# Kernel tuning notes

Measured on AMD Instinct MI355X. Metric: run time of the kernel, lower is better.

The kernel has to match this reference:

```python
import jax, jax.numpy as jnp
import numpy as np

N = 50000          # nodes
E = 800000         # edges (avg degree 16)
F = 128            # in_dim = num_hidden*heads = pred_dim
H = 4              # attention heads per layer
D = 32             # num_hidden (per-head dim)
R = 11             # rel_num
L = 2              # num_layers
SCALE = float(1.0 / np.sqrt(D))


def setup_inputs() -> dict:
    key = jax.random.key(0)
    ks = jax.random.split(key, 16)
    inputs = jax.random.normal(ks[0], (N, F), jnp.float32)
    edge_types = jax.random.randint(ks[1], (E,), 0, R)
    src = jax.random.randint(ks[2], (E,), 0, N)
    dst = jax.random.randint(ks[3], (E,), 0, N)
    centrality = jax.random.uniform(ks[4], (N,), jnp.float32)
    rel_emb = jax.random.normal(ks[5], (R, F), jnp.float32) * 0.1
    # stacked per-layer projection weights (both layers have F -> H*D = F)
    Wq = jax.random.normal(ks[6], (L, F, H * D), jnp.float32) * 0.05
    Wk = jax.random.normal(ks[7], (L, F, H * D), jnp.float32) * 0.05
    Wv = jax.random.normal(ks[8], (L, F, H * D), jnp.float32) * 0.05
    We = jax.random.normal(ks[9], (L, F, H * D), jnp.float32) * 0.05
    bq = jnp.zeros((L, H * D), jnp.float32)
    bk = jnp.zeros((L, H * D), jnp.float32)
    bv = jnp.zeros((L, H * D), jnp.float32)
    be = jnp.zeros((L, H * D), jnp.float32)
    W_out = jax.random.normal(ks[10], (H * D, 1), jnp.float32) * 0.05
    b_out = jnp.zeros((1,), jnp.float32)
    gamma = jnp.ones((1,), jnp.float32)
    beta = jnp.zeros((1,), jnp.float32)
    return {"inputs": inputs, "edge_types": edge_types, "src": src, "dst": dst,
            "centrality": centrality, "rel_emb": rel_emb,
            "Wq": Wq, "bq": bq, "Wk": Wk, "bk": bk, "Wv": Wv, "bv": bv,
            "We": We, "be": be, "W_out": W_out, "b_out": b_out,
            "gamma": gamma, "beta": beta}


def _segment_softmax(score, dst, n):
    # score: [E, H]; softmax over incoming edges of each dst node
    m = jax.ops.segment_max(score, dst, num_segments=n)          # [N, H]
    ex = jnp.exp(score - m[dst])                                  # [E, H]
    s = jax.ops.segment_sum(ex, dst, num_segments=n)              # [N, H]
    return ex / (s[dst] + 1e-9)


def reference(inputs, edge_types, src, dst, centrality, rel_emb,
              Wq, bq, Wk, bk, Wv, bv, We, be, W_out, b_out, gamma, beta):
    h = inputs                                   # [N, F]
    ef = rel_emb[edge_types]                     # [E, pred_dim] relational edge embedding
    for l in range(L):
        q = (h @ Wq[l] + bq[l]).reshape(N, H, D)
        k = (h @ Wk[l] + bk[l]).reshape(N, H, D)
        v = (h @ Wv[l] + bv[l]).reshape(N, H, D)
        e = (ef @ We[l] + be[l]).reshape(E, H, D)
        # edge_mode="add": edge features added to keys/values on each edge
        ke = k[src] + e                           # [E, H, D]
        score = jnp.sum(q[dst] * ke, axis=-1) * SCALE   # [E, H]
        attn = _segment_softmax(score, dst, N)          # [E, H]
        msg = attn[:, :, None] * (v[src] + e)           # [E, H, D]
        agg = jax.ops.segment_sum(msg, dst, num_segments=N)  # [N, H, D]
        # identity residual (in_dim == H*D) + ELU activation
        h = jax.nn.elu(agg.reshape(N, H * D) + h)
    logits = h @ W_out + b_out                    # [N, 1]
    logits = jax.nn.relu((centrality * gamma + beta)[:, None] * logits)
    return logits
```

## Files before the change

kernel.cpp:

```cpp
#include <hip/hip_runtime.h>
#include <hip/hip_bf16.h>
#include <math.h>

#define SCALE_C 0.17677669529663687f
#define CAPP 64

typedef short bf16x8 __attribute__((ext_vector_type(8)));
typedef float f32x4 __attribute__((ext_vector_type(4)));


__global__ __launch_bounds__(256) void prep_scatter_k(
    const float* __restrict__ Wq, const float* __restrict__ Wk, const float* __restrict__ Wv,
    __hip_bfloat16* __restrict__ wf,
    const float* __restrict__ rel_emb, const float* __restrict__ We, const float* __restrict__ be,
    float* __restrict__ re, int R, int reb,
    const int* __restrict__ dst, const int* __restrict__ src, const int* __restrict__ etype,
    int E, int* __restrict__ cnt, int* __restrict__ bins) {
  int b = blockIdx.x;
  if (b < 48) {
    int tid = b * 256 + threadIdx.x;
    int lane = tid & 63;
    int frag = tid >> 6;
    int ks = frag & 3;
    int ct = (frag >> 2) & 7;
    int mat = frag >> 5;
    int l = mat / 3, m = mat % 3;
    const float* W = ((m == 0) ? Wq : (m == 1) ? Wk : Wv) + (size_t)l * 128 * 128;
    int nn = ct * 16 + (lane & 15);
    int k0 = ks * 32 + (lane >> 4) * 8;
    __hip_bfloat16 tmp[8];
    #pragma unroll
    for (int j = 0; j < 8; ++j) tmp[j] = __float2bfloat16(W[(size_t)(k0 + j) * 128 + nn]);
    *(uint4*)&wf[(size_t)frag * 64 * 8 + (size_t)lane * 8] = *(const uint4*)tmp;
  } else if (b < 48 + reb) {
    int idx = (b - 48) * 256 + threadIdx.x;
    int tot = 2 * R * 128;
    if (idx >= tot) return;
    int c = idx & 127;
    int r = (idx >> 7) % R;
    int l = idx / (R * 128);
    const float* W = We + (size_t)l * 128 * 128;
    float acc = be[l * 128 + c];
    #pragma unroll 4
    for (int kk = 0; kk < 128; ++kk) acc += rel_emb[r * 128 + kk] * W[kk * 128 + c];
    re[idx] = acc;
  } else {
    int e = (b - 48 - reb) * 256 + threadIdx.x;
    if (e < E) {
      int d = dst[e];
      int pos = atomicAdd(&cnt[d], 1);
      if (pos < CAPP) bins[(d << 6) + pos] = src[e] | (etype[e] << 20);
    }
  }
}


__device__ __forceinline__ void qkv_body(
    const float* __restrict__ Xf, const __hip_bfloat16* __restrict__ Xb,
    const __hip_bfloat16* __restrict__ wf,
    const float* __restrict__ bq, const float* __restrict__ bk, const float* __restrict__ bv,
    __hip_bfloat16* __restrict__ qo, __hip_bfloat16* __restrict__ kvo, int n, int bid) {
  __shared__ __hip_bfloat16 kvt[2][32][264];
  int wid = threadIdx.x >> 6;
  int lane = threadIdx.x & 63;
  int row0 = bid * 64 + wid * 32;
  if (row0 >= n) return;
  int cl = lane & 15;
  int quad = lane >> 4;

  bf16x8 afrag[2][4];
  #pragma unroll
  for (int s = 0; s < 2; ++s) {
    int arow = row0 + s * 16 + cl;
    bool av = arow < n;
    if (Xb) {
      const __hip_bfloat16* xr = Xb + (size_t)arow * 128 + quad * 8;
      #pragma unroll
      for (int ks = 0; ks < 4; ++ks) {
        uint4 raw = av ? *(const uint4*)(xr + ks * 32) : make_uint4(0, 0, 0, 0);
        afrag[s][ks] = __builtin_bit_cast(bf16x8, raw);
      }
    } else {
      const float* xr = Xf + (size_t)arow * 128 + quad * 8;
      #pragma unroll
      for (int ks = 0; ks < 4; ++ks) {
        float4 x0 = av ? *(const float4*)(xr + ks * 32)     : make_float4(0.f, 0.f, 0.f, 0.f);
        float4 x1 = av ? *(const float4*)(xr + ks * 32 + 4) : make_float4(0.f, 0.f, 0.f, 0.f);
        union { bf16x8 v; __hip_bfloat16 h[8]; } fu;
        fu.h[0] = __float2bfloat16(x0.x); fu.h[1] = __float2bfloat16(x0.y);
        fu.h[2] = __float2bfloat16(x0.z); fu.h[3] = __float2bfloat16(x0.w);
        fu.h[4] = __float2bfloat16(x1.x); fu.h[5] = __float2bfloat16(x1.y);
        fu.h[6] = __float2bfloat16(x1.z); fu.h[7] = __float2bfloat16(x1.w);
        afrag[s][ks] = fu.v;
      }
    }
  }
  const uint4* wfu = (const uint4*)wf;

  #pragma unroll
  for (int ct = 0; ct < 8; ++ct) {
    f32x4 a0 = {0.f, 0.f, 0.f, 0.f}, a1 = {0.f, 0.f, 0.f, 0.f};
    #pragma unroll
    for (int ks = 0; ks < 4; ++ks) {
      uint4 braw = wfu[((size_t)ct * 4 + ks) * 64 + lane];
      bf16x8 bfr = __builtin_bit_cast(bf16x8, braw);
      a0 = __builtin_amdgcn_mfma_f32_16x16x32_bf16(afrag[0][ks], bfr, a0, 0, 0, 0);
      a1 = __builtin_amdgcn_mfma_f32_16x16x32_bf16(afrag[1][ks], bfr, a1, 0, 0, 0);
    }
    int c = ct * 16 + cl;
    float bb = bq[c];
    #pragma unroll
    for (int r = 0; r < 4; ++r) {
      kvt[wid][quad * 4 + r][c]      = __float2bfloat16((a0[r] + bb) * SCALE_C);
      kvt[wid][16 + quad * 4 + r][c] = __float2bfloat16((a1[r] + bb) * SCALE_C);
    }
  }
  {
    const uint4* tsrc = (const uint4*)&kvt[wid][0][0];
    #pragma unroll
    for (int it = 0; it < 8; ++it) {
      int idx = it * 64 + lane;
      int row = idx >> 4, g = idx & 15;
      if (row0 + row < n)
        *(uint4*)&qo[((size_t)(row0 + row)) * 128 + g * 8] = tsrc[row * 33 + g];
    }
  }

  #pragma unroll
  for (int m = 1; m <= 2; ++m) {
    const float* bias = (m == 1) ? bk : bv;
    #pragma unroll
    for (int ct = 0; ct < 8; ++ct) {
      f32x4 a0 = {0.f, 0.f, 0.f, 0.f}, a1 = {0.f, 0.f, 0.f, 0.f};
      #pragma unroll
      for (int ks = 0; ks < 4; ++ks) {
        uint4 braw = wfu[((size_t)(m * 8 + ct) * 4 + ks) * 64 + lane];
        bf16x8 bfr = __builtin_bit_cast(bf16x8, braw);
        a0 = __builtin_amdgcn_mfma_f32_16x16x32_bf16(afrag[0][ks], bfr, a0, 0, 0, 0);
        a1 = __builtin_amdgcn_mfma_f32_16x16x32_bf16(afrag[1][ks], bfr, a1, 0, 0, 0);
      }
      int c = ct * 16 + cl;
      float bb = bias[c];
      int p = 8 * (c >> 2) + (c & 3) + ((m == 2) ? 4 : 0);
      #pragma unroll
      for (int r = 0; r < 4; ++r) {
        kvt[wid][quad * 4 + r][p]      = __float2bfloat16(a0[r] + bb);
        kvt[wid][16 + quad * 4 + r][p] = __float2bfloat16(a1[r] + bb);
      }
    }
  }
  {
    const uint4* tsrc = (const uint4*)&kvt[wid][0][0];
    #pragma unroll
    for (int it = 0; it < 16; ++it) {
      int idx = it * 64 + lane;
      int row = idx >> 5, off = idx & 31;
      if (row0 + row < n)
        *(uint4*)&kvo[((size_t)(row0 + row)) * 256 + off * 8] = tsrc[row * 33 + off];
    }
  }
}

__global__ __launch_bounds__(128) void qkv1_k(
    const float* __restrict__ Xf, const __hip_bfloat16* __restrict__ wf,
    const float* __restrict__ bq, const float* __restrict__ bk, const float* __restrict__ bv,
    __hip_bfloat16* __restrict__ qo, __hip_bfloat16* __restrict__ kvo, int n) {
  qkv_body(Xf, nullptr, wf, bq, bk, bv, qo, kvo, n, blockIdx.x);
}

__global__ __launch_bounds__(128) void qkv2_k(
    const __hip_bfloat16* __restrict__ Xb, const __hip_bfloat16* __restrict__ wf,
    const float* __restrict__ bq, const float* __restrict__ bk, const float* __restrict__ bv,
    __hip_bfloat16* __restrict__ qo, __hip_bfloat16* __restrict__ kvo, int n) {
  qkv_body(nullptr, Xb, wf, bq, bk, bv, qo, kvo, n, blockIdx.x);
}


__global__ __launch_bounds__(256) void edge_k(
    const __hip_bfloat16* __restrict__ qb, const __hip_bfloat16* __restrict__ kv,
    const float* __restrict__ re,
    const int* __restrict__ bins, const int* __restrict__ cnt,
    const float* __restrict__ h_in_f, const __hip_bfloat16* __restrict__ h_in_b,
    __hip_bfloat16* __restrict__ h_out_b,
    const float* __restrict__ Wout, const float* __restrict__ bout,
    const float* __restrict__ cent, const float* __restrict__ gamma,
    const float* __restrict__ beta, float* __restrict__ outp, int n) {
  int node = blockIdx.x * 4 + (threadIdx.x >> 6);
  if (node >= n) return;
  int lane = threadIdx.x & 63;
  int j = lane & 15;
  int quarter = lane >> 4;
  int rs = node << 6;
  int deg = cnt[node];
  deg = deg < CAPP ? deg : CAPP;

  uint4 qraw = *((const uint4*)(qb + ((size_t)node << 7)) + j);
  float qa0 = __uint_as_float(qraw.x << 16), qa1 = __uint_as_float(qraw.x & 0xffff0000u);
  float qa2 = __uint_as_float(qraw.y << 16), qa3 = __uint_as_float(qraw.y & 0xffff0000u);
  float qa4 = __uint_as_float(qraw.z << 16), qa5 = __uint_as_float(qraw.z & 0xffff0000u);
  float qa6 = __uint_as_float(qraw.w << 16), qa7 = __uint_as_float(qraw.w & 0xffff0000u);

  float ssum = 0.f;
  float acc0 = 0.f, acc1 = 0.f, acc2 = 0.f, acc3 = 0.f;
  float acc4 = 0.f, acc5 = 0.f, acc6 = 0.f, acc7 = 0.f;
  int nit = (deg + 3) >> 2;

  int pk1 = (quarter < deg) ? bins[rs + quarter] : 0;
  int pk2 = (quarter + 4 < deg) ? bins[rs + quarter + 4] : 0;
  uint s0 = (uint)pk1 & 0xFFFFFu, t0 = (uint)pk1 >> 20;
  const uint4* kr0 = (const uint4*)kv + (s0 * 32u + (uint)(j * 2));
  uint4 raw0 = kr0[0];
  uint4 raw1 = kr0[1];
  const float4* rr0 = (const float4*)re + (t0 * 32u + (uint)(j * 2));
  float4 r0 = rr0[0];
  float4 r1 = rr0[1];
  pk1 = pk2;

  for (int i = 0; i < nit; ++i) {
    int e2 = 4 * (i + 2) + quarter;
    pk2 = (e2 < deg) ? bins[rs + e2] : 0;
    uint s1 = (uint)pk1 & 0xFFFFFu, t1 = (uint)pk1 >> 20;
    const uint4* krn = (const uint4*)kv + (s1 * 32u + (uint)(j * 2));
    uint4 nraw0 = krn[0];
    uint4 nraw1 = krn[1];
    const float4* rrn = (const float4*)re + (t1 * 32u + (uint)(j * 2));
    float4 nr0 = rrn[0];
    float4 nr1 = rrn[1];

    bool valid = 4 * i + quarter < deg;
    float k0 = __uint_as_float(raw0.x << 16);
    float k1 = __uint_as_float(raw0.x & 0xffff0000u);
    float k2 = __uint_as_float(raw0.y << 16);
    float k3 = __uint_as_float(raw0.y & 0xffff0000u);
    float v0 = __uint_as_float(raw0.z << 16);
    float v1 = __uint_as_float(raw0.z & 0xffff0000u);
    float v2 = __uint_as_float(raw0.w << 16);
    float v3 = __uint_as_float(raw0.w & 0xffff0000u);
    float k4 = __uint_as_float(raw1.x << 16);
    float k5 = __uint_as_float(raw1.x & 0xffff0000u);
    float k6 = __uint_as_float(raw1.y << 16);
    float k7 = __uint_as_float(raw1.y & 0xffff0000u);
    float v4 = __uint_as_float(raw1.z << 16);
    float v5 = __uint_as_float(raw1.z & 0xffff0000u);
    float v6 = __uint_as_float(raw1.w << 16);
    float v7 = __uint_as_float(raw1.w & 0xffff0000u);
    float p = qa0 * (k0 + r0.x) + qa1 * (k1 + r0.y) + qa2 * (k2 + r0.z) + qa3 * (k3 + r0.w)
            + qa4 * (k4 + r1.x) + qa5 * (k5 + r1.y) + qa6 * (k6 + r1.z) + qa7 * (k7 + r1.w);
    p += __shfl_xor(p, 1);
    p += __shfl_xor(p, 2);
    float w = valid ? __expf(p) : 0.f;
    ssum += w;
    acc0 += w * (v0 + r0.x);
    acc1 += w * (v1 + r0.y);
    acc2 += w * (v2 + r0.z);
    acc3 += w * (v3 + r0.w);
    acc4 += w * (v4 + r1.x);
    acc5 += w * (v5 + r1.y);
    acc6 += w * (v6 + r1.z);
    acc7 += w * (v7 + r1.w);

    raw0 = nraw0; raw1 = nraw1; r0 = nr0; r1 = nr1;
    pk1 = pk2;
  }
  ssum += __shfl_xor(ssum, 16); ssum += __shfl_xor(ssum, 32);
  acc0 += __shfl_xor(acc0, 16); acc0 += __shfl_xor(acc0, 32);
  acc1 += __shfl_xor(acc1, 16); acc1 += __shfl_xor(acc1, 32);
  acc2 += __shfl_xor(acc2, 16); acc2 += __shfl_xor(acc2, 32);
  acc3 += __shfl_xor(acc3, 16); acc3 += __shfl_xor(acc3, 32);
  acc4 += __shfl_xor(acc4, 16); acc4 += __shfl_xor(acc4, 32);
  acc5 += __shfl_xor(acc5, 16); acc5 += __shfl_xor(acc5, 32);
  acc6 += __shfl_xor(acc6, 16); acc6 += __shfl_xor(acc6, 32);
  acc7 += __shfl_xor(acc7, 16); acc7 += __shfl_xor(acc7, 32);
  if (quarter != 0) return;

  float inv = 1.f / (ssum + 1e-9f);
  float4 h0, h1;
  if (h_in_b) {
    uint4 hraw = *((const uint4*)(h_in_b + ((size_t)node << 7)) + j);
    h0.x = __uint_as_float(hraw.x << 16); h0.y = __uint_as_float(hraw.x & 0xffff0000u);
    h0.z = __uint_as_float(hraw.y << 16); h0.w = __uint_as_float(hraw.y & 0xffff0000u);
    h1.x = __uint_as_float(hraw.z << 16); h1.y = __uint_as_float(hraw.z & 0xffff0000u);
    h1.z = __uint_as_float(hraw.w << 16); h1.w = __uint_as_float(hraw.w & 0xffff0000u);
  } else {
    const float4* hrow = (const float4*)h_in_f + ((uint)node * 32u + (uint)(j * 2));
    h0 = hrow[0]; h1 = hrow[1];
  }
  float x0 = acc0 * inv + h0.x;
  float x1 = acc1 * inv + h0.y;
  float x2 = acc2 * inv + h0.z;
  float x3 = acc3 * inv + h0.w;
  float x4 = acc4 * inv + h1.x;
  float x5 = acc5 * inv + h1.y;
  float x6 = acc6 * inv + h1.z;
  float x7 = acc7 * inv + h1.w;
  x0 = x0 > 0.f ? x0 : expm1f(x0);
  x1 = x1 > 0.f ? x1 : expm1f(x1);
  x2 = x2 > 0.f ? x2 : expm1f(x2);
  x3 = x3 > 0.f ? x3 : expm1f(x3);
  x4 = x4 > 0.f ? x4 : expm1f(x4);
  x5 = x5 > 0.f ? x5 : expm1f(x5);
  x6 = x6 > 0.f ? x6 : expm1f(x6);
  x7 = x7 > 0.f ? x7 : expm1f(x7);
  if (outp == nullptr) {
    union { uint4 u; __hip_bfloat16 hh[8]; } P;
    P.hh[0] = __float2bfloat16(x0); P.hh[1] = __float2bfloat16(x1);
    P.hh[2] = __float2bfloat16(x2); P.hh[3] = __float2bfloat16(x3);
    P.hh[4] = __float2bfloat16(x4); P.hh[5] = __float2bfloat16(x5);
    P.hh[6] = __float2bfloat16(x6); P.hh[7] = __float2bfloat16(x7);
    *((uint4*)(h_out_b + ((size_t)node << 7)) + j) = P.u;
  } else {
    const float4* wrow = (const float4*)Wout + (uint)(j * 2);
    float4 w0 = wrow[0], w1 = wrow[1];
    float pp = x0 * w0.x + x1 * w0.y + x2 * w0.z + x3 * w0.w
             + x4 * w1.x + x5 * w1.y + x6 * w1.z + x7 * w1.w;
    pp += __shfl_xor(pp, 1);
    pp += __shfl_xor(pp, 2);
    pp += __shfl_xor(pp, 4);
    pp += __shfl_xor(pp, 8);
    if (lane == 0) {
      float lg = pp + bout[0];
      lg *= (cent[node] * gamma[0] + beta[0]);
      outp[node] = fmaxf(lg, 0.f);
    }
  }
}


extern "C" void kernel_launch(void* const* d_in, const int* in_sizes, int n_in,
                              void* d_out, int out_size, void* d_ws, size_t ws_size,
                              hipStream_t stream) {
  const float* inputs  = (const float*)d_in[0];
  const int*   etype   = (const int*)d_in[1];
  const int*   src     = (const int*)d_in[2];
  const int*   dst     = (const int*)d_in[3];
  const float* cent    = (const float*)d_in[4];
  const float* rel_emb = (const float*)d_in[5];
  const float* Wq      = (const float*)d_in[6];
  const float* bq      = (const float*)d_in[7];
  const float* Wk      = (const float*)d_in[8];
  const float* bk      = (const float*)d_in[9];
  const float* Wv      = (const float*)d_in[10];
  const float* bv      = (const float*)d_in[11];
  const float* We      = (const float*)d_in[12];
  const float* be      = (const float*)d_in[13];
  const float* Wout    = (const float*)d_in[14];
  const float* bout    = (const float*)d_in[15];
  const float* gamma   = (const float*)d_in[16];
  const float* beta    = (const float*)d_in[17];
  float* out = (float*)d_out;

  const int N = in_sizes[0] / 128;
  const int E = in_sizes[1];
  const int R = in_sizes[5] / 128;

  float* re = (float*)d_ws;
  __hip_bfloat16* hb = (__hip_bfloat16*)(re + 2 * (size_t)R * 128);
  __hip_bfloat16* qb = hb + (size_t)N * 128;
  __hip_bfloat16* kv = qb + (size_t)N * 128;
  __hip_bfloat16* wf = kv + (size_t)N * 256;
  int* cnt  = (int*)(wf + 6 * 16384);
  int* bins = cnt + N;

  hipMemsetAsync(cnt, 0, (size_t)N * sizeof(int), stream);

  int reb = (2 * R * 128 + 255) / 256;
  int SB  = (E + 255) / 256;
  prep_scatter_k<<<48 + reb + SB, 256, 0, stream>>>(Wq, Wk, Wv, wf, rel_emb, We, be, re, R, reb,
                                                    dst, src, etype, E, cnt, bins);

  int QB = (N + 63) / 64;
  int eb = (N + 3) / 4;
  qkv1_k<<<QB, 128, 0, stream>>>(inputs, wf, bq, bk, bv, qb, kv, N);
  edge_k<<<eb, 256, 0, stream>>>(qb, kv, re, bins, cnt,
                                 inputs, nullptr, hb,
                                 Wout, bout, cent, gamma, beta, nullptr, N);
  qkv2_k<<<QB, 128, 0, stream>>>(hb, wf + (size_t)3 * 16384,
                                 bq + 128, bk + 128, bv + 128, qb, kv, N);
  edge_k<<<eb, 256, 0, stream>>>(qb, kv, re + (size_t)R * 128, bins, cnt,
                                 nullptr, hb, nullptr,
                                 Wout, bout, cent, gamma, beta, out, N);
}
```

Before: 309.3 us.

## Fuse QKV and edge stages into one persistent cooperative kernel with grid syncs

Replaces the four separate qkv/edge launches with a single persistent cooperative kernel. Waves loop over work items and the stages are separated by grid.sync, which removes the launch gaps and tail effects between kernels. The QKV shared-memory tile is halved to 16 rows per wave, with the second half held in registers, so that more blocks fit per CU. In exchange, grid-wide barriers become a cost, register pressure goes up, and persistent scheduling may load-balance the variable-degree edge work worse.

```diff
diff --git a/kernel.cpp b/kernel.cpp
--- a/kernel.cpp
+++ b/kernel.cpp
@@ -1,6 +1,9 @@
 #include <hip/hip_runtime.h>
+#include <hip/hip_cooperative_groups.h>
 #include <hip/hip_bf16.h>
 #include <math.h>
+
+namespace cg = cooperative_groups;
 
 #define SCALE_C 0.17677669529663687f
 #define CAPP 64
@@ -55,15 +58,14 @@
 }
 
 
-__device__ __forceinline__ void qkv_body(
+__device__ __forceinline__ void qkv_wave(
     const float* __restrict__ Xf, const __hip_bfloat16* __restrict__ Xb,
     const __hip_bfloat16* __restrict__ wf,
     const float* __restrict__ bq, const float* __restrict__ bk, const float* __restrict__ bv,
-    __hip_bfloat16* __restrict__ qo, __hip_bfloat16* __restrict__ kvo, int n, int bid) {
-  __shared__ __hip_bfloat16 kvt[2][32][264];
-  int wid = threadIdx.x >> 6;
+    __hip_bfloat16* __restrict__ qo, __hip_bfloat16* __restrict__ kvo, int n, int item,
+    __hip_bfloat16 (*tile)[264]) {
   int lane = threadIdx.x & 63;
-  int row0 = bid * 64 + wid * 32;
+  int row0 = item * 32;
   if (row0 >= n) return;
   int cl = lane & 15;
   int quad = lane >> 4;
@@ -96,7 +98,9 @@
     }
   }
   const uint4* wfu = (const uint4*)wf;
-
+  const uint4* ts = (const uint4*)&tile[0][0];
+
+  float holdq[8][4];
   #pragma unroll
   for (int ct = 0; ct < 8; ++ct) {
     f32x4 a0 = {0.f, 0.f, 0.f, 0.f}, a1 = {0.f, 0.f, 0.f, 0.f};
@@ -111,21 +115,34 @@
     float bb = bq[c];
     #pragma unroll
     for (int r = 0; r < 4; ++r) {
-      kvt[wid][quad * 4 + r][c]      = __float2bfloat16((a0[r] + bb) * SCALE_C);
-      kvt[wid][16 + quad * 4 + r][c] = __float2bfloat16((a1[r] + bb) * SCALE_C);
-    }
-  }
-  {
-    const uint4* tsrc = (const uint4*)&kvt[wid][0][0];
-    #pragma unroll
-    for (int it = 0; it < 8; ++it) {
-      int idx = it * 64 + lane;
-      int row = idx >> 4, g = idx & 15;
-      if (row0 + row < n)
-        *(uint4*)&qo[((size_t)(row0 + row)) * 128 + g * 8] = tsrc[row * 33 + g];
-    }
-  }
-
+      tile[quad * 4 + r][c] = __float2bfloat16((a0[r] + bb) * SCALE_C);
+      holdq[ct][r] = a1[r];
+    }
+  }
+  #pragma unroll
+  for (int it = 0; it < 4; ++it) {
+    int idx = it * 64 + lane;
+    int row = idx >> 4, gcol = idx & 15;
+    if (row0 + row < n)
+      *(uint4*)&qo[((size_t)(row0 + row)) * 128 + gcol * 8] = ts[row * 33 + gcol];
+  }
+  #pragma unroll
+  for (int ct = 0; ct < 8; ++ct) {
+    int c = ct * 16 + cl;
+    float bb = bq[c];
+    #pragma unroll
+    for (int r = 0; r < 4; ++r)
+      tile[quad * 4 + r][c] = __float2bfloat16((holdq[ct][r] + bb) * SCALE_C);
+  }
+  #pragma unroll
+  for (int it = 0; it < 4; ++it) {
+    int idx = it * 64 + lane;
+    int row = idx >> 4, gcol = idx & 15;
+    if (row0 + 16 + row < n)
+      *(uint4*)&qo[((size_t)(row0 + 16 + row)) * 128 + gcol * 8] = ts[row * 33 + gcol];
+  }
+
+  float holdk[8][4], holdv[8][4];
   #pragma unroll
   for (int m = 1; m <= 2; ++m) {
     const float* bias = (m == 1) ? bk : bv;
@@ -144,39 +161,42 @@
       int p = 8 * (c >> 2) + (c & 3) + ((m == 2) ? 4 : 0);
       #pragma unroll
       for (int r = 0; r < 4; ++r) {
-        kvt[wid][quad * 4 + r][p]      = __float2bfloat16(a0[r] + bb);
-        kvt[wid][16 + quad * 4 + r][p] = __float2bfloat16(a1[r] + bb);
+        tile[quad * 4 + r][p] = __float2bfloat16(a0[r] + bb);
+        if (m == 1) holdk[ct][r] = a1[r]; else holdv[ct][r] = a1[r];
       }
     }
   }
-  {
-    const uint4* tsrc = (const uint4*)&kvt[wid][0][0];
-    #pragma unroll
-    for (int it = 0; it < 16; ++it) {
-      int idx = it * 64 + lane;
-      int row = idx >> 5, off = idx & 31;
-      if (row0 + row < n)
-        *(uint4*)&kvo[((size_t)(row0 + row)) * 256 + off * 8] = tsrc[row * 33 + off];
-    }
+  #pragma unroll
+  for (int it = 0; it < 8; ++it) {
+    int idx = it * 64 + lane;
+    int row = idx >> 5, off = idx & 31;
+    if (row0 + row < n)
+      *(uint4*)&kvo[((size_t)(row0 + row)) * 256 + off * 8] = ts[row * 33 + off];
+  }
+  #pragma unroll
+  for (int m = 1; m <= 2; ++m) {
+    const float* bias = (m == 1) ? bk : bv;
+    #pragma unroll
+    for (int ct = 0; ct < 8; ++ct) {
+      int c = ct * 16 + cl;
+      float bb = bias[c];
+      int p = 8 * (c >> 2) + (c & 3) + ((m == 2) ? 4 : 0);
+      #pragma unroll
+      for (int r = 0; r < 4; ++r)
+        tile[quad * 4 + r][p] = __float2bfloat16(((m == 1) ? holdk[ct][r] : holdv[ct][r]) + bb);
+    }
+  }
+  #pragma unroll
+  for (int it = 0; it < 8; ++it) {
+    int idx = it * 64 + lane;
+    int row = idx >> 5, off = idx & 31;
+    if (row0 + 16 + row < n)
+      *(uint4*)&kvo[((size_t)(row0 + 16 + row)) * 256 + off * 8] = ts[row * 33 + off];
   }
 }
 
-__global__ __launch_bounds__(128) void qkv1_k(
-    const float* __restrict__ Xf, const __hip_bfloat16* __restrict__ wf,
-    const float* __restrict__ bq, const float* __restrict__ bk, const float* __restrict__ bv,
-    __hip_bfloat16* __restrict__ qo, __hip_bfloat16* __restrict__ kvo, int n) {
-  qkv_body(Xf, nullptr, wf, bq, bk, bv, qo, kvo, n, blockIdx.x);
-}
-
-__global__ __launch_bounds__(128) void qkv2_k(
-    const __hip_bfloat16* __restrict__ Xb, const __hip_bfloat16* __restrict__ wf,
-    const float* __restrict__ bq, const float* __restrict__ bk, const float* __restrict__ bv,
-    __hip_bfloat16* __restrict__ qo, __hip_bfloat16* __restrict__ kvo, int n) {
-  qkv_body(nullptr, Xb, wf, bq, bk, bv, qo, kvo, n, blockIdx.x);
-}
-
-
-__global__ __launch_bounds__(256) void edge_k(
+
+__device__ __forceinline__ void edge_body(
     const __hip_bfloat16* __restrict__ qb, const __hip_bfloat16* __restrict__ kv,
     const float* __restrict__ re,
     const int* __restrict__ bins, const int* __restrict__ cnt,
@@ -184,8 +204,8 @@
     __hip_bfloat16* __restrict__ h_out_b,
     const float* __restrict__ Wout, const float* __restrict__ bout,
     const float* __restrict__ cent, const float* __restrict__ gamma,
-    const float* __restrict__ beta, float* __restrict__ outp, int n) {
-  int node = blockIdx.x * 4 + (threadIdx.x >> 6);
+    const float* __restrict__ beta, float* __restrict__ outp, int n, int item) {
+  int node = item * 4 + (threadIdx.x >> 6);
   if (node >= n) return;
   int lane = threadIdx.x & 63;
   int j = lane & 15;
@@ -326,6 +346,45 @@
 }
 
 
+struct MegaP {
+  const float* inputs;
+  const __hip_bfloat16* wf;
+  const float* bq; const float* bk; const float* bv;
+  __hip_bfloat16* hb; __hip_bfloat16* qb; __hip_bfloat16* kv;
+  const float* re1; const float* re2;
+  const int* bins; const int* cnt;
+  const float* Wout; const float* bout; const float* cent;
+  const float* gamma; const float* beta;
+  float* out; int n;
+};
+
+__global__ __launch_bounds__(256, 4) void mega_k(MegaP P) {
+  cg::grid_group grid = cg::this_grid();
+  __shared__ __hip_bfloat16 tile[4][16][264];
+  int wid = threadIdx.x >> 6;
+  int gw = blockIdx.x * 4 + wid;
+  int GW = gridDim.x * 4;
+  int n = P.n;
+  int QI = (n + 31) >> 5;
+  int EI = (n + 3) >> 2;
+
+  for (int it = gw; it < QI; it += GW)
+    qkv_wave(P.inputs, nullptr, P.wf, P.bq, P.bk, P.bv, P.qb, P.kv, n, it, tile[wid]);
+  grid.sync();
+  for (int it = blockIdx.x; it < EI; it += gridDim.x)
+    edge_body(P.qb, P.kv, P.re1, P.bins, P.cnt, P.inputs, nullptr, P.hb,
+              P.Wout, P.bout, P.cent, P.gamma, P.beta, nullptr, n, it);
+  grid.sync();
+  for (int it = gw; it < QI; it += GW)
+    qkv_wave(nullptr, P.hb, P.wf + (size_t)3 * 16384, P.bq + 128, P.bk + 128, P.bv + 128,
+             P.qb, P.kv, n, it, tile[wid]);
+  grid.sync();
+  for (int it = blockIdx.x; it < EI; it += gridDim.x)
+    edge_body(P.qb, P.kv, P.re2, P.bins, P.cnt, nullptr, P.hb, nullptr,
+              P.Wout, P.bout, P.cent, P.gamma, P.beta, P.out, n, it);
+}
+
+
 extern "C" void kernel_launch(void* const* d_in, const int* in_sizes, int n_in,
                               void* d_out, int out_size, void* d_ws, size_t ws_size,
                               hipStream_t stream) {
@@ -368,15 +427,27 @@
   prep_scatter_k<<<48 + reb + SB, 256, 0, stream>>>(Wq, Wk, Wv, wf, rel_emb, We, be, re, R, reb,
                                                     dst, src, etype, E, cnt, bins);
 
-  int QB = (N + 63) / 64;
-  int eb = (N + 3) / 4;
-  qkv1_k<<<QB, 128, 0, stream>>>(inputs, wf, bq, bk, bv, qb, kv, N);
-  edge_k<<<eb, 256, 0, stream>>>(qb, kv, re, bins, cnt,
-                                 inputs, nullptr, hb,
-                                 Wout, bout, cent, gamma, beta, nullptr, N);
-  qkv2_k<<<QB, 128, 0, stream>>>(hb, wf + (size_t)3 * 16384,
-                                 bq + 128, bk + 128, bv + 128, qb, kv, N);
-  edge_k<<<eb, 256, 0, stream>>>(qb, kv, re + (size_t)R * 128, bins, cnt,
-                                 nullptr, hb, nullptr,
-                                 Wout, bout, cent, gamma, beta, out, N);
+  int perCU = 0;
+  hipOccupancyMaxActiveBlocksPerMultiprocessor(&perCU, (const void*)mega_k, 256, 0);
+  if (perCU <= 0) perCU = 4;
+  int dev = 0, nCU = 256;
+  hipGetDevice(&dev);
+  hipDeviceGetAttribute(&nCU, hipDeviceAttributeMultiprocessorCount, dev);
+  long long cap = (long long)perCU * nCU;
+  if (cap > 4096) cap = 4096;
+  int G = (int)cap;
+  int EI = (N + 3) / 4;
+  if (G > EI) G = EI;
+  if (G < 1) G = 1;
+
+  MegaP P;
+  P.inputs = inputs; P.wf = wf;
+  P.bq = bq; P.bk = bk; P.bv = bv;
+  P.hb = hb; P.qb = qb; P.kv = kv;
+  P.re1 = re; P.re2 = re + (size_t)R * 128;
+  P.bins = bins; P.cnt = cnt;
+  P.Wout = Wout; P.bout = bout; P.cent = cent; P.gamma = gamma; P.beta = beta;
+  P.out = out; P.n = N;
+  void* kargs[] = { (void*)&P };
+  hipLaunchCooperativeKernel((const void*)mega_k, dim3(G), dim3(256), kargs, 0, stream);
 }
```

Measured after the change: 766.1 us. 148% more time.

## Make edge kernel persistent with next-node prefetch; vectorize scatter to 4 edges/thread

Applied to the files above, without the earlier changes.

The edge attention kernel becomes a grid-stride loop in which each wavefront handles about four nodes. While it computes the current node, it prefetches the next node's degree, query row and first bin entries, hiding the latency of dependent loads between nodes. The scatter phase now has each thread load four edges with int4 vector loads and issue four atomics, which cuts thread count and load instructions. Fewer waves launched may reduce latency hiding, and the int4 loads assume the index arrays are 16-byte aligned.

```diff
diff --git a/kernel.cpp b/kernel.cpp
--- a/kernel.cpp
+++ b/kernel.cpp
@@ -45,11 +45,26 @@
     for (int kk = 0; kk < 128; ++kk) acc += rel_emb[r * 128 + kk] * W[kk * 128 + c];
     re[idx] = acc;
   } else {
-    int e = (b - 48 - reb) * 256 + threadIdx.x;
-    if (e < E) {
-      int d = dst[e];
-      int pos = atomicAdd(&cnt[d], 1);
-      if (pos < CAPP) bins[(d << 6) + pos] = src[e] | (etype[e] << 20);
+    int t4 = (b - 48 - reb) * 256 + threadIdx.x;
+    int base = t4 * 4;
+    if (base + 3 < E) {
+      int4 d4 = *(const int4*)(dst + base);
+      int4 s4 = *(const int4*)(src + base);
+      int4 e4 = *(const int4*)(etype + base);
+      int p0 = atomicAdd(&cnt[d4.x], 1);
+      int p1 = atomicAdd(&cnt[d4.y], 1);
+      int p2 = atomicAdd(&cnt[d4.z], 1);
+      int p3 = atomicAdd(&cnt[d4.w], 1);
+      if (p0 < CAPP) bins[(d4.x << 6) + p0] = s4.x | (e4.x << 20);
+      if (p1 < CAPP) bins[(d4.y << 6) + p1] = s4.y | (e4.y << 20);
+      if (p2 < CAPP) bins[(d4.z << 6) + p2] = s4.z | (e4.z << 20);
+      if (p3 < CAPP) bins[(d4.w << 6) + p3] = s4.w | (e4.w << 20);
+    } else {
+      for (int e = base; e < E; ++e) {
+        int d = dst[e];
+        int pos = atomicAdd(&cnt[d], 1);
+        if (pos < CAPP) bins[(d << 6) + pos] = src[e] | (etype[e] << 20);
+      }
     }
   }
 }
@@ -185,143 +200,162 @@
     const float* __restrict__ Wout, const float* __restrict__ bout,
     const float* __restrict__ cent, const float* __restrict__ gamma,
     const float* __restrict__ beta, float* __restrict__ outp, int n) {
-  int node = blockIdx.x * 4 + (threadIdx.x >> 6);
-  if (node >= n) return;
+  int wgid = blockIdx.x * 4 + (threadIdx.x >> 6);
+  if (wgid >= n) return;
+  int GW = gridDim.x * 4;
   int lane = threadIdx.x & 63;
   int j = lane & 15;
   int quarter = lane >> 4;
-  int rs = node << 6;
-  int deg = cnt[node];
-  deg = deg < CAPP ? deg : CAPP;
-
+
+  int node = wgid;
+  int deg0 = cnt[node];
   uint4 qraw = *((const uint4*)(qb + ((size_t)node << 7)) + j);
-  float qa0 = __uint_as_float(qraw.x << 16), qa1 = __uint_as_float(qraw.x & 0xffff0000u);
-  float qa2 = __uint_as_float(qraw.y << 16), qa3 = __uint_as_float(qraw.y & 0xffff0000u);
-  float qa4 = __uint_as_float(qraw.z << 16), qa5 = __uint_as_float(qraw.z & 0xffff0000u);
-  float qa6 = __uint_as_float(qraw.w << 16), qa7 = __uint_as_float(qraw.w & 0xffff0000u);
-
-  float ssum = 0.f;
-  float acc0 = 0.f, acc1 = 0.f, acc2 = 0.f, acc3 = 0.f;
-  float acc4 = 0.f, acc5 = 0.f, acc6 = 0.f, acc7 = 0.f;
-  int nit = (deg + 3) >> 2;
-
-  int pk1 = (quarter < deg) ? bins[rs + quarter] : 0;
-  int pk2 = (quarter + 4 < deg) ? bins[rs + quarter + 4] : 0;
-  uint s0 = (uint)pk1 & 0xFFFFFu, t0 = (uint)pk1 >> 20;
-  const uint4* kr0 = (const uint4*)kv + (s0 * 32u + (uint)(j * 2));
-  uint4 raw0 = kr0[0];
-  uint4 raw1 = kr0[1];
-  const float4* rr0 = (const float4*)re + (t0 * 32u + (uint)(j * 2));
-  float4 r0 = rr0[0];
-  float4 r1 = rr0[1];
-  pk1 = pk2;
-
-  for (int i = 0; i < nit; ++i) {
-    int e2 = 4 * (i + 2) + quarter;
-    pk2 = (e2 < deg) ? bins[rs + e2] : 0;
-    uint s1 = (uint)pk1 & 0xFFFFFu, t1 = (uint)pk1 >> 20;
-    const uint4* krn = (const uint4*)kv + (s1 * 32u + (uint)(j * 2));
-    uint4 nraw0 = krn[0];
-    uint4 nraw1 = krn[1];
-    const float4* rrn = (const float4*)re + (t1 * 32u + (uint)(j * 2));
-    float4 nr0 = rrn[0];
-    float4 nr1 = rrn[1];
-
-    bool valid = 4 * i + quarter < deg;
-    float k0 = __uint_as_float(raw0.x << 16);
-    float k1 = __uint_as_float(raw0.x & 0xffff0000u);
-    float k2 = __uint_as_float(raw0.y << 16);
-    float k3 = __uint_as_float(raw0.y & 0xffff0000u);
-    float v0 = __uint_as_float(raw0.z << 16);
-    float v1 = __uint_as_float(raw0.z & 0xffff0000u);
-    float v2 = __uint_as_float(raw0.w << 16);
-    float v3 = __uint_as_float(raw0.w & 0xffff0000u);
-    float k4 = __uint_as_float(raw1.x << 16);
-    float k5 = __uint_as_float(raw1.x & 0xffff0000u);
-    float k6 = __uint_as_float(raw1.y << 16);
-    float k7 = __uint_as_float(raw1.y & 0xffff0000u);
-    float v4 = __uint_as_float(raw1.z << 16);
-    float v5 = __uint_as_float(raw1.z & 0xffff0000u);
-    float v6 = __uint_as_float(raw1.w << 16);
-    float v7 = __uint_as_float(raw1.w & 0xffff0000u);
-    float p = qa0 * (k0 + r0.x) + qa1 * (k1 + r0.y) + qa2 * (k2 + r0.z) + qa3 * (k3 + r0.w)
-            + qa4 * (k4 + r1.x) + qa5 * (k5 + r1.y) + qa6 * (k6 + r1.z) + qa7 * (k7 + r1.w);
-    p += __shfl_xor(p, 1);
-    p += __shfl_xor(p, 2);
-    float w = valid ? __expf(p) : 0.f;
-    ssum += w;
-    acc0 += w * (v0 + r0.x);
-    acc1 += w * (v1 + r0.y);
-    acc2 += w * (v2 + r0.z);
-    acc3 += w * (v3 + r0.w);
-    acc4 += w * (v4 + r1.x);
-    acc5 += w * (v5 + r1.y);
-    acc6 += w * (v6 + r1.z);
-    acc7 += w * (v7 + r1.w);
-
-    raw0 = nraw0; raw1 = nraw1; r0 = nr0; r1 = nr1;
+  int pka = bins[(node << 6) + quarter];
+  int pkb = bins[(node << 6) + quarter + 4];
+
+  while (true) {
+    int nnode = node + GW;
+    bool hasnext = nnode < n;
+    int pnode = hasnext ? nnode : node;
+    int ndeg = cnt[pnode];
+    uint4 nqraw = *((const uint4*)(qb + ((size_t)pnode << 7)) + j);
+    int npka = bins[(pnode << 6) + quarter];
+    int npkb = bins[(pnode << 6) + quarter + 4];
+
+    int deg = deg0 < CAPP ? deg0 : CAPP;
+    int rs = node << 6;
+    float qa0 = __uint_as_float(qraw.x << 16), qa1 = __uint_as_float(qraw.x & 0xffff0000u);
+    float qa2 = __uint_as_float(qraw.y << 16), qa3 = __uint_as_float(qraw.y & 0xffff0000u);
+    float qa4 = __uint_as_float(qraw.z << 16), qa5 = __uint_as_float(qraw.z & 0xffff0000u);
+    float qa6 = __uint_as_float(qraw.w << 16), qa7 = __uint_as_float(qraw.w & 0xffff0000u);
+
+    float ssum = 0.f;
+    float acc0 = 0.f, acc1 = 0.f, acc2 = 0.f, acc3 = 0.f;
+    float acc4 = 0.f, acc5 = 0.f, acc6 = 0.f, acc7 = 0.f;
+    int nit = (deg + 3) >> 2;
+
+    int pk1 = (quarter < deg) ? pka : 0;
+    int pk2 = (quarter + 4 < deg) ? pkb : 0;
+    uint s0 = (uint)pk1 & 0xFFFFFu, t0 = (uint)pk1 >> 20;
+    const uint4* kr0 = (const uint4*)kv + (s0 * 32u + (uint)(j * 2));
+    uint4 raw0 = kr0[0];
+    uint4 raw1 = kr0[1];
+    const float4* rr0 = (const float4*)re + (t0 * 32u + (uint)(j * 2));
+    float4 r0 = rr0[0];
+    float4 r1 = rr0[1];
     pk1 = pk2;
-  }
-  ssum += __shfl_xor(ssum, 16); ssum += __shfl_xor(ssum, 32);
-  acc0 += __shfl_xor(acc0, 16); acc0 += __shfl_xor(acc0, 32);
-  acc1 += __shfl_xor(acc1, 16); acc1 += __shfl_xor(acc1, 32);
-  acc2 += __shfl_xor(acc2, 16); acc2 += __shfl_xor(acc2, 32);
-  acc3 += __shfl_xor(acc3, 16); acc3 += __shfl_xor(acc3, 32);
-  acc4 += __shfl_xor(acc4, 16); acc4 += __shfl_xor(acc4, 32);
-  acc5 += __shfl_xor(acc5, 16); acc5 += __shfl_xor(acc5, 32);
-  acc6 += __shfl_xor(acc6, 16); acc6 += __shfl_xor(acc6, 32);
-  acc7 += __shfl_xor(acc7, 16); acc7 += __shfl_xor(acc7, 32);
-  if (quarter != 0) return;
-
-  float inv = 1.f / (ssum + 1e-9f);
-  float4 h0, h1;
-  if (h_in_b) {
-    uint4 hraw = *((const uint4*)(h_in_b + ((size_t)node << 7)) + j);
-    h0.x = __uint_as_float(hraw.x << 16); h0.y = __uint_as_float(hraw.x & 0xffff0000u);
-    h0.z = __uint_as_float(hraw.y << 16); h0.w = __uint_as_float(hraw.y & 0xffff0000u);
-    h1.x = __uint_as_float(hraw.z << 16); h1.y = __uint_as_float(hraw.z & 0xffff0000u);
-    h1.z = __uint_as_float(hraw.w << 16); h1.w = __uint_as_float(hraw.w & 0xffff0000u);
-  } else {
-    const float4* hrow = (const float4*)h_in_f + ((uint)node * 32u + (uint)(j * 2));
-    h0 = hrow[0]; h1 = hrow[1];
-  }
-  float x0 = acc0 * inv + h0.x;
-  float x1 = acc1 * inv + h0.y;
-  float x2 = acc2 * inv + h0.z;
-  float x3 = acc3 * inv + h0.w;
-  float x4 = acc4 * inv + h1.x;
-  float x5 = acc5 * inv + h1.y;
-  float x6 = acc6 * inv + h1.z;
-  float x7 = acc7 * inv + h1.w;
-  x0 = x0 > 0.f ? x0 : expm1f(x0);
-  x1 = x1 > 0.f ? x1 : expm1f(x1);
-  x2 = x2 > 0.f ? x2 : expm1f(x2);
-  x3 = x3 > 0.f ? x3 : expm1f(x3);
-  x4 = x4 > 0.f ? x4 : expm1f(x4);
-  x5 = x5 > 0.f ? x5 : expm1f(x5);
-  x6 = x6 > 0.f ? x6 : expm1f(x6);
-  x7 = x7 > 0.f ? x7 : expm1f(x7);
-  if (outp == nullptr) {
-    union { uint4 u; __hip_bfloat16 hh[8]; } P;
-    P.hh[0] = __float2bfloat16(x0); P.hh[1] = __float2bfloat16(x1);
-    P.hh[2] = __float2bfloat16(x2); P.hh[3] = __float2bfloat16(x3);
-    P.hh[4] = __float2bfloat16(x4); P.hh[5] = __float2bfloat16(x5);
-    P.hh[6] = __float2bfloat16(x6); P.hh[7] = __float2bfloat16(x7);
-    *((uint4*)(h_out_b + ((size_t)node << 7)) + j) = P.u;
-  } else {
-    const float4* wrow = (const float4*)Wout + (uint)(j * 2);
-    float4 w0 = wrow[0], w1 = wrow[1];
-    float pp = x0 * w0.x + x1 * w0.y + x2 * w0.z + x3 * w0.w
-             + x4 * w1.x + x5 * w1.y + x6 * w1.z + x7 * w1.w;
-    pp += __shfl_xor(pp, 1);
-    pp += __shfl_xor(pp, 2);
-    pp += __shfl_xor(pp, 4);
-    pp += __shfl_xor(pp, 8);
-    if (lane == 0) {
-      float lg = pp + bout[0];
-      lg *= (cent[node] * gamma[0] + beta[0]);
-      outp[node] = fmaxf(lg, 0.f);
-    }
+
+    for (int i = 0; i < nit; ++i) {
+      int e2 = 4 * (i + 2) + quarter;
+      pk2 = (e2 < deg) ? bins[rs + e2] : 0;
+      uint s1 = (uint)pk1 & 0xFFFFFu, t1 = (uint)pk1 >> 20;
+      const uint4* krn = (const uint4*)kv + (s1 * 32u + (uint)(j * 2));
+      uint4 nraw0 = krn[0];
+      uint4 nraw1 = krn[1];
+      const float4* rrn = (const float4*)re + (t1 * 32u + (uint)(j * 2));
+      float4 nr0 = rrn[0];
+      float4 nr1 = rrn[1];
+
+      bool valid = 4 * i + quarter < deg;
+      float k0 = __uint_as_float(raw0.x << 16);
+      float k1 = __uint_as_float(raw0.x & 0xffff0000u);
+      float k2 = __uint_as_float(raw0.y << 16);
+      float k3 = __uint_as_float(raw0.y & 0xffff0000u);
+      float v0 = __uint_as_float(raw0.z << 16);
+      float v1 = __uint_as_float(raw0.z & 0xffff0000u);
+      float v2 = __uint_as_float(raw0.w << 16);
+      float v3 = __uint_as_float(raw0.w & 0xffff0000u);
+      float k4 = __uint_as_float(raw1.x << 16);
+      float k5 = __uint_as_float(raw1.x & 0xffff0000u);
+      float k6 = __uint_as_float(raw1.y << 16);
+      float k7 = __uint_as_float(raw1.y & 0xffff0000u);
+      float v4 = __uint_as_float(raw1.z << 16);
+      float v5 = __uint_as_float(raw1.z & 0xffff0000u);
+      float v6 = __uint_as_float(raw1.w << 16);
+      float v7 = __uint_as_float(raw1.w & 0xffff0000u);
+      float p = qa0 * (k0 + r0.x) + qa1 * (k1 + r0.y) + qa2 * (k2 + r0.z) + qa3 * (k3 + r0.w)
+              + qa4 * (k4 + r1.x) + qa5 * (k5 + r1.y) + qa6 * (k6 + r1.z) + qa7 * (k7 + r1.w);
+      p += __shfl_xor(p, 1);
+      p += __shfl_xor(p, 2);
+      float w = valid ? __expf(p) : 0.f;
+      ssum += w;
+      acc0 += w * (v0 + r0.x);
+      acc1 += w * (v1 + r0.y);
+      acc2 += w * (v2 + r0.z);
+      acc3 += w * (v3 + r0.w);
+      acc4 += w * (v4 + r1.x);
+      acc5 += w * (v5 + r1.y);
+      acc6 += w * (v6 + r1.z);
+      acc7 += w * (v7 + r1.w);
+
+      raw0 = nraw0; raw1 = nraw1; r0 = nr0; r1 = nr1;
+      pk1 = pk2;
+    }
+    ssum += __shfl_xor(ssum, 16); ssum += __shfl_xor(ssum, 32);
+    acc0 += __shfl_xor(acc0, 16); acc0 += __shfl_xor(acc0, 32);
+    acc1 += __shfl_xor(acc1, 16); acc1 += __shfl_xor(acc1, 32);
+    acc2 += __shfl_xor(acc2, 16); acc2 += __shfl_xor(acc2, 32);
+    acc3 += __shfl_xor(acc3, 16); acc3 += __shfl_xor(acc3, 32);
+    acc4 += __shfl_xor(acc4, 16); acc4 += __shfl_xor(acc4, 32);
+    acc5 += __shfl_xor(acc5, 16); acc5 += __shfl_xor(acc5, 32);
+    acc6 += __shfl_xor(acc6, 16); acc6 += __shfl_xor(acc6, 32);
+    acc7 += __shfl_xor(acc7, 16); acc7 += __shfl_xor(acc7, 32);
+
+    if (quarter == 0) {
+      float inv = 1.f / (ssum + 1e-9f);
+      float4 h0, h1;
+      if (h_in_b) {
+        uint4 hraw = *((const uint4*)(h_in_b + ((size_t)node << 7)) + j);
+        h0.x = __uint_as_float(hraw.x << 16); h0.y = __uint_as_float(hraw.x & 0xffff0000u);
+        h0.z = __uint_as_float(hraw.y << 16); h0.w = __uint_as_float(hraw.y & 0xffff0000u);
+        h1.x = __uint_as_float(hraw.z << 16); h1.y = __uint_as_float(hraw.z & 0xffff0000u);
+        h1.z = __uint_as_float(hraw.w << 16); h1.w = __uint_as_float(hraw.w & 0xffff0000u);
+      } else {
+        const float4* hrow = (const float4*)h_in_f + ((uint)node * 32u + (uint)(j * 2));
+        h0 = hrow[0]; h1 = hrow[1];
+      }
+      float x0 = acc0 * inv + h0.x;
+      float x1 = acc1 * inv + h0.y;
+      float x2 = acc2 * inv + h0.z;
+      float x3 = acc3 * inv + h0.w;
+      float x4 = acc4 * inv + h1.x;
+      float x5 = acc5 * inv + h1.y;
+      float x6 = acc6 * inv + h1.z;
+      float x7 = acc7 * inv + h1.w;
+      x0 = x0 > 0.f ? x0 : expm1f(x0);
+      x1 = x1 > 0.f ? x1 : expm1f(x1);
+      x2 = x2 > 0.f ? x2 : expm1f(x2);
+      x3 = x3 > 0.f ? x3 : expm1f(x3);
+      x4 = x4 > 0.f ? x4 : expm1f(x4);
+      x5 = x5 > 0.f ? x5 : expm1f(x5);
+      x6 = x6 > 0.f ? x6 : expm1f(x6);
+      x7 = x7 > 0.f ? x7 : expm1f(x7);
+      if (outp == nullptr) {
+        union { uint4 u; __hip_bfloat16 hh[8]; } P;
+        P.hh[0] = __float2bfloat16(x0); P.hh[1] = __float2bfloat16(x1);
+        P.hh[2] = __float2bfloat16(x2); P.hh[3] = __float2bfloat16(x3);
+        P.hh[4] = __float2bfloat16(x4); P.hh[5] = __float2bfloat16(x5);
+        P.hh[6] = __float2bfloat16(x6); P.hh[7] = __float2bfloat16(x7);
+        *((uint4*)(h_out_b + ((size_t)node << 7)) + j) = P.u;
+      } else {
+        const float4* wrow = (const float4*)Wout + (uint)(j * 2);
+        float4 w0 = wrow[0], w1 = wrow[1];
+        float pp = x0 * w0.x + x1 * w0.y + x2 * w0.z + x3 * w0.w
+                 + x4 * w1.x + x5 * w1.y + x6 * w1.z + x7 * w1.w;
+        pp += __shfl_xor(pp, 1);
+        pp += __shfl_xor(pp, 2);
+        pp += __shfl_xor(pp, 4);
+        pp += __shfl_xor(pp, 8);
+        if (lane == 0) {
+          float lg = pp + bout[0];
+          lg *= (cent[node] * gamma[0] + beta[0]);
+          outp[node] = fmaxf(lg, 0.f);
+        }
+      }
+    }
+
+    if (!hasnext) break;
+    node = nnode; deg0 = ndeg; qraw = nqraw; pka = npka; pkb = npkb;
   }
 }
 
@@ -364,12 +398,12 @@
   hipMemsetAsync(cnt, 0, (size_t)N * sizeof(int), stream);
 
   int reb = (2 * R * 128 + 255) / 256;
-  int SB  = (E + 255) / 256;
+  int SB  = ((E + 3) / 4 + 255) / 256;
   prep_scatter_k<<<48 + reb + SB, 256, 0, stream>>>(Wq, Wk, Wv, wf, rel_emb, We, be, re, R, reb,
                                                     dst, src, etype, E, cnt, bins);
 
   int QB = (N + 63) / 64;
-  int eb = (N + 3) / 4;
+  int eb = (N + 15) / 16;
   qkv1_k<<<QB, 128, 0, stream>>>(inputs, wf, bq, bk, bv, qb, kv, N);
   edge_k<<<eb, 256, 0, stream>>>(qb, kv, re, bins, cnt,
                                  inputs, nullptr, hb,
```

Result: slower. 320.4 us (+3.6%).
